# Optimization experiments

Hardware: AMD Instinct MI355X
Metric: run time of the kernel (lower is better)

The kernel has to match this reference:

```python
import jax, jax.numpy as jnp
import numpy as np

# Keyed conv layer as structured SpMM in affine coordinates.
# W (N x N sparse, N = C*H*W + 1) stored in ELL format: for each output row r,
# cols[r, :] are the K column indices and vals[r, :] the nonzero values.
C, H, W_, KS = 32, 32, 32, 3
N = C * H * W_ + 1          # 32769, homogeneous (+1 bias) dim
K = C * KS * KS             # 288 nnz per row (Toeplitz conv structure)
B = 32                      # batch


def setup_inputs() -> dict:
    key = jax.random.key(0)
    k1, k2, k3 = jax.random.split(key, 3)
    x_affine = jax.random.normal(k1, (B, N), dtype=jnp.float32)
    cols = jax.random.randint(k2, (N, K), 0, N, dtype=jnp.int32)
    vals = jax.random.normal(k3, (N, K), dtype=jnp.float32) / np.float32(np.sqrt(K))
    return {"x_affine": x_affine, "vals": vals, "cols": cols}


def reference(x_affine, vals, cols):
    # y = (W @ x_affine^T)^T  with W in row-wise ELL format.
    # Gather input features addressed by each row's nonzero columns, then
    # contract over the K nonzeros of each row.
    xg = x_affine[:, cols]                      # [B, N, K] gathered features
    y = jnp.einsum('bnk,nk->bn', xg, vals)      # [B, N]
    return y
```

## Files before the change

### kernel.cpp

```cpp
#include <hip/hip_runtime.h>

constexpr int B = 32;
constexpr int N = 32 * 32 * 32 + 1;
constexpr int K = 32 * 3 * 3;

using i4 = __attribute__((ext_vector_type(4))) int;
using f4 = __attribute__((ext_vector_type(4))) float;
using h4 = __attribute__((ext_vector_type(4))) _Float16;

__global__ __launch_bounds__(256) void transpose_x_f16_kernel(
    const float* __restrict__ x, _Float16* __restrict__ xT) {
  __shared__ float tile[32][33];
  const int n0 = blockIdx.x * 32;
  const int t  = threadIdx.x;
  const int lb = t & 31;
  const int lr = t >> 5;
#pragma unroll
  for (int i = 0; i < 4; ++i) {
    const int b = lr + i * 8;
    const int n = n0 + lb;
    float v = 0.f;
    if (n < N) v = x[(size_t)b * N + n];
    tile[lb][b] = v;
  }
  __syncthreads();
#pragma unroll
  for (int i = 0; i < 4; ++i) {
    const int nl = lr + i * 8;
    const int n  = n0 + nl;
    if (n < N) xT[(size_t)n * B + lb] = (_Float16)tile[nl][lb];
  }
}

__global__ __launch_bounds__(256, 8) void gather_dot_f16_u16_kernel(
    const _Float16* __restrict__ xT, const float* __restrict__ vals,
    const int* __restrict__ cols, float* __restrict__ yT) {
  __shared__ unsigned short scols[32 * K];
  const int t    = threadIdx.x;
  const int lane = t & 63;
  const int wave = t >> 6;
  const int g    = lane >> 3;
  const int bq   = lane & 7;
  const int n0   = blockIdx.x * 32;

  {
    const long long last = (long long)N * K - 4;
    unsigned int* sc32 = (unsigned int*)scols;
#pragma unroll
    for (int r = 0; r < 9; ++r) {
      const int c = r * 256 + t;
      long long gi = (long long)n0 * K + (long long)c * 4;
      if (gi > last) gi = last;
      const i4 w = *reinterpret_cast<const i4*>(cols + gi);
      const unsigned int p0 = (unsigned int)(w.x & 0xFFFF) | ((unsigned int)w.y << 16);
      const unsigned int p1 = (unsigned int)(w.z & 0xFFFF) | ((unsigned int)w.w << 16);
      sc32[c * 2]     = p0;
      sc32[c * 2 + 1] = p1;
    }
  }
  __syncthreads();

  const int nl = wave * 8 + g;
  const int n  = n0 + nl;
  if (n >= N) return;

  const unsigned short* __restrict__ srow = scols + nl * K;
  const char* __restrict__ xTb  = (const char*)xT + bq * 8;
  const char* __restrict__ vrow = (const char*)(vals + (size_t)n * K);

  f4 acc0 = {0.f, 0.f, 0.f, 0.f};
  f4 acc1 = {0.f, 0.f, 0.f, 0.f};

  const int rot = g * 8;

#pragma unroll 4
  for (int k = 0; k < K; k += 8) {
    int kk = k + rot;
    if (kk >= K) kk -= K;

    const i4 cp = *reinterpret_cast<const i4*>(srow + kk);
    const f4 v0 = *reinterpret_cast<const f4*>(vrow + kk * 4);
    const f4 v1 = *reinterpret_cast<const f4*>(vrow + kk * 4 + 16);

    const unsigned int w0 = (unsigned int)cp.x;
    const unsigned int w1 = (unsigned int)cp.y;
    const unsigned int w2 = (unsigned int)cp.z;
    const unsigned int w3 = (unsigned int)cp.w;
    const unsigned int o0 = (w0 << 6) & 0x3FFFC0u;
    const unsigned int o1 = (w0 >> 10) & 0x3FFFC0u;
    const unsigned int o2 = (w1 << 6) & 0x3FFFC0u;
    const unsigned int o3 = (w1 >> 10) & 0x3FFFC0u;
    const unsigned int o4 = (w2 << 6) & 0x3FFFC0u;
    const unsigned int o5 = (w2 >> 10) & 0x3FFFC0u;
    const unsigned int o6 = (w3 << 6) & 0x3FFFC0u;
    const unsigned int o7 = (w3 >> 10) & 0x3FFFC0u;

    const h4 x0 = *reinterpret_cast<const h4*>(xTb + o0);
    const h4 x1 = *reinterpret_cast<const h4*>(xTb + o1);
    const h4 x2 = *reinterpret_cast<const h4*>(xTb + o2);
    const h4 x3 = *reinterpret_cast<const h4*>(xTb + o3);
    const h4 x4 = *reinterpret_cast<const h4*>(xTb + o4);
    const h4 x5 = *reinterpret_cast<const h4*>(xTb + o5);
    const h4 x6 = *reinterpret_cast<const h4*>(xTb + o6);
    const h4 x7 = *reinterpret_cast<const h4*>(xTb + o7);

    acc0 += __builtin_convertvector(x0, f4) * v0.x;
    acc0 += __builtin_convertvector(x1, f4) * v0.y;
    acc0 += __builtin_convertvector(x2, f4) * v0.z;
    acc0 += __builtin_convertvector(x3, f4) * v0.w;
    acc1 += __builtin_convertvector(x4, f4) * v1.x;
    acc1 += __builtin_convertvector(x5, f4) * v1.y;
    acc1 += __builtin_convertvector(x6, f4) * v1.z;
    acc1 += __builtin_convertvector(x7, f4) * v1.w;
  }

  acc0 += acc1;
  *reinterpret_cast<f4*>(yT + (size_t)n * B + bq * 4) = acc0;
}

__global__ __launch_bounds__(256) void transpose_y_kernel(
    const float* __restrict__ yT, float* __restrict__ y) {
  __shared__ float tile[32][33];
  const int n0 = blockIdx.x * 32;
  const int t  = threadIdx.x;
  const int lb = t & 31;
  const int lr = t >> 5;
#pragma unroll
  for (int i = 0; i < 4; ++i) {
    const int nl = lr + i * 8;
    const int n  = n0 + nl;
    float v = 0.f;
    if (n < N) v = yT[(size_t)n * B + lb];
    tile[nl][lb] = v;
  }
  __syncthreads();
#pragma unroll
  for (int i = 0; i < 4; ++i) {
    const int b = lr + i * 8;
    const int n = n0 + lb;
    if (n < N) y[(size_t)b * N + n] = tile[lb][b];
  }
}

__global__ __launch_bounds__(256) void gather_dot_fallback(
    const float* __restrict__ x, const float* __restrict__ vals,
    const int* __restrict__ cols, float* __restrict__ y) {
  const int t    = threadIdx.x;
  const int lane = t & 63;
  const int wave = t >> 6;
  const int g    = lane >> 3;
  const int bq   = lane & 7;
  const int n    = blockIdx.x * 32 + wave * 8 + g;
  if (n >= N) return;
  const int*   crow = cols + (size_t)n * K;
  const float* vrow = vals + (size_t)n * K;
  float4 acc = make_float4(0.f, 0.f, 0.f, 0.f);
  for (int k = 0; k < K; ++k) {
    const int   c = crow[k];
    const float v = vrow[k];
    acc.x += x[(size_t)(bq * 4 + 0) * N + c] * v;
    acc.y += x[(size_t)(bq * 4 + 1) * N + c] * v;
    acc.z += x[(size_t)(bq * 4 + 2) * N + c] * v;
    acc.w += x[(size_t)(bq * 4 + 3) * N + c] * v;
  }
  y[(size_t)(bq * 4 + 0) * N + n] = acc.x;
  y[(size_t)(bq * 4 + 1) * N + n] = acc.y;
  y[(size_t)(bq * 4 + 2) * N + n] = acc.z;
  y[(size_t)(bq * 4 + 3) * N + n] = acc.w;
}

extern "C" void kernel_launch(void* const* d_in, const int* in_sizes, int n_in,
                              void* d_out, int out_size, void* d_ws, size_t ws_size,
                              hipStream_t stream) {
  const float* x    = (const float*)d_in[0];
  const float* vals = (const float*)d_in[1];
  const int*   cols = (const int*)d_in[2];
  float*       y    = (float*)d_out;

  const size_t nb       = (size_t)N * B;
  const size_t xT_bytes = nb * sizeof(_Float16);
  const size_t need     = xT_bytes + nb * sizeof(float);

  const int nblocks = (N + 31) / 32;

  if (ws_size >= need) {
    _Float16* xT = (_Float16*)d_ws;
    float*    yT = (float*)((char*)d_ws + xT_bytes);
    transpose_x_f16_kernel<<<nblocks, 256, 0, stream>>>(x, xT);
    gather_dot_f16_u16_kernel<<<nblocks, 256, 0, stream>>>(xT, vals, cols, yT);
    transpose_y_kernel<<<nblocks, 256, 0, stream>>>(yT, y);
  } else {
    gather_dot_fallback<<<nblocks, 256, 0, stream>>>(x, vals, cols, y);
  }
}
```

Measured before the change: 173.4 us.

## Split K dimension across two blocks and sum partials in output transpose

```diff
diff --git a/kernel.cpp b/kernel.cpp
--- a/kernel.cpp
+++ b/kernel.cpp
@@ -3,6 +3,7 @@
 constexpr int B = 32;
 constexpr int N = 32 * 32 * 32 + 1;
 constexpr int K = 32 * 3 * 3;
+constexpr int KH = K / 2;
 
 using i4 = __attribute__((ext_vector_type(4))) int;
 using f4 = __attribute__((ext_vector_type(4))) float;
@@ -32,24 +33,28 @@
   }
 }
 
-__global__ __launch_bounds__(256, 8) void gather_dot_f16_u16_kernel(
+__global__ __launch_bounds__(256, 8) void gather_dot_f16_u16_ks2_kernel(
     const _Float16* __restrict__ xT, const float* __restrict__ vals,
     const int* __restrict__ cols, float* __restrict__ yT) {
-  __shared__ unsigned short scols[32 * K];
+  __shared__ unsigned short scols[32 * KH];
   const int t    = threadIdx.x;
   const int lane = t & 63;
   const int wave = t >> 6;
   const int g    = lane >> 3;
   const int bq   = lane & 7;
   const int n0   = blockIdx.x * 32;
+  const int q    = blockIdx.y;
+  const int k0   = q * KH;
 
   {
     const long long last = (long long)N * K - 4;
     unsigned int* sc32 = (unsigned int*)scols;
 #pragma unroll
-    for (int r = 0; r < 9; ++r) {
-      const int c = r * 256 + t;
-      long long gi = (long long)n0 * K + (long long)c * 4;
+    for (int r = 0; r < 4; ++r) {
+      const int c   = r * 256 + t;
+      const int row = c / 36;
+      const int off = c - row * 36;
+      long long gi = (long long)(n0 + row) * K + k0 + (long long)off * 4;
       if (gi > last) gi = last;
       const i4 w = *reinterpret_cast<const i4*>(cols + gi);
       const unsigned int p0 = (unsigned int)(w.x & 0xFFFF) | ((unsigned int)w.y << 16);
@@ -57,6 +62,18 @@
       sc32[c * 2]     = p0;
       sc32[c * 2 + 1] = p1;
     }
+    if (t < 128) {
+      const int c   = 1024 + t;
+      const int row = c / 36;
+      const int off = c - row * 36;
+      long long gi = (long long)(n0 + row) * K + k0 + (long long)off * 4;
+      if (gi > last) gi = last;
+      const i4 w = *reinterpret_cast<const i4*>(cols + gi);
+      const unsigned int p0 = (unsigned int)(w.x & 0xFFFF) | ((unsigned int)w.y << 16);
+      const unsigned int p1 = (unsigned int)(w.z & 0xFFFF) | ((unsigned int)w.w << 16);
+      sc32[c * 2]     = p0;
+      sc32[c * 2 + 1] = p1;
+    }
   }
   __syncthreads();
 
@@ -64,9 +81,9 @@
   const int n  = n0 + nl;
   if (n >= N) return;
 
-  const unsigned short* __restrict__ srow = scols + nl * K;
+  const unsigned short* __restrict__ srow = scols + nl * KH;
   const char* __restrict__ xTb  = (const char*)xT + bq * 8;
-  const char* __restrict__ vrow = (const char*)(vals + (size_t)n * K);
+  const char* __restrict__ vrow = (const char*)(vals + (size_t)n * K + k0);
 
   f4 acc0 = {0.f, 0.f, 0.f, 0.f};
   f4 acc1 = {0.f, 0.f, 0.f, 0.f};
@@ -74,9 +91,9 @@
   const int rot = g * 8;
 
 #pragma unroll 4
-  for (int k = 0; k < K; k += 8) {
+  for (int k = 0; k < KH; k += 8) {
     int kk = k + rot;
-    if (kk >= K) kk -= K;
+    if (kk >= KH) kk -= KH;
 
     const i4 cp = *reinterpret_cast<const i4*>(srow + kk);
     const f4 v0 = *reinterpret_cast<const f4*>(vrow + kk * 4);
@@ -115,22 +132,26 @@
   }
 
   acc0 += acc1;
-  *reinterpret_cast<f4*>(yT + (size_t)n * B + bq * 4) = acc0;
-}
-
-__global__ __launch_bounds__(256) void transpose_y_kernel(
+  *reinterpret_cast<f4*>(yT + (size_t)q * N * B + (size_t)n * B + bq * 4) = acc0;
+}
+
+__global__ __launch_bounds__(256) void transpose_y_sum2_kernel(
     const float* __restrict__ yT, float* __restrict__ y) {
   __shared__ float tile[32][33];
   const int n0 = blockIdx.x * 32;
   const int t  = threadIdx.x;
   const int lb = t & 31;
   const int lr = t >> 5;
+  constexpr size_t NB = (size_t)N * B;
 #pragma unroll
   for (int i = 0; i < 4; ++i) {
     const int nl = lr + i * 8;
     const int n  = n0 + nl;
     float v = 0.f;
-    if (n < N) v = yT[(size_t)n * B + lb];
+    if (n < N) {
+      const size_t idx = (size_t)n * B + lb;
+      v = yT[idx] + yT[NB + idx];
+    }
     tile[nl][lb] = v;
   }
   __syncthreads();
@@ -179,7 +200,7 @@
 
   const size_t nb       = (size_t)N * B;
   const size_t xT_bytes = nb * sizeof(_Float16);
-  const size_t need     = xT_bytes + nb * sizeof(float);
+  const size_t need     = xT_bytes + 2 * nb * sizeof(float);
 
   const int nblocks = (N + 31) / 32;
 
@@ -187,8 +208,9 @@
     _Float16* xT = (_Float16*)d_ws;
     float*    yT = (float*)((char*)d_ws + xT_bytes);
     transpose_x_f16_kernel<<<nblocks, 256, 0, stream>>>(x, xT);
-    gather_dot_f16_u16_kernel<<<nblocks, 256, 0, stream>>>(xT, vals, cols, yT);
-    transpose_y_kernel<<<nblocks, 256, 0, stream>>>(yT, y);
+    dim3 grid(nblocks, 2);
+    gather_dot_f16_u16_ks2_kernel<<<grid, 256, 0, stream>>>(xT, vals, cols, yT);
+    transpose_y_sum2_kernel<<<nblocks, 256, 0, stream>>>(yT, y);
   } else {
     gather_dot_fallback<<<nblocks, 256, 0, stream>>>(x, vals, cols, y);
   }
```

Measured after the change: 178.3 us. +2.9%, slower.
